# Kernel tuning notes

Measured on AMD Instinct MI355X. Metric: run time of the kernel, lower is better.

The kernel has to match this reference:

```python
import jax, jax.numpy as jnp
import numpy as np

B, T_ENC, D = 64, 512, 256
MEL, R = 80, 5
T_DEC = 200
IN = MEL * R  # 400


def _p(key, shape, scale):
    return jax.random.normal(key, shape, dtype=jnp.float32) * scale


def setup_inputs() -> dict:
    key = jax.random.key(0)
    ks = jax.random.split(key, 32)
    s = lambda fan: 1.0 / np.sqrt(fan)
    inp = {
        "enc_out": jax.random.normal(ks[0], (B, T_ENC, D), dtype=jnp.float32),
        "mel_in": jax.random.normal(ks[1], (B, T_DEC, IN), dtype=jnp.float32),
        # prenet: 400 -> 256 -> 128
        "prenet_w1": _p(ks[2], (IN, 256), s(IN)), "prenet_b1": jnp.zeros((256,), jnp.float32),
        "prenet_w2": _p(ks[3], (256, 128), s(256)), "prenet_b2": jnp.zeros((128,), jnp.float32),
        # attention GRUCell: input 128+256=384, hidden 256 (torch gate order r,z,n)
        "att_w_ih": _p(ks[4], (384, 768), s(384)), "att_w_hh": _p(ks[5], (256, 768), s(256)),
        "att_b_ih": jnp.zeros((768,), jnp.float32), "att_b_hh": jnp.zeros((768,), jnp.float32),
        # Bahdanau attention
        "mem_w": _p(ks[6], (D, 256), s(D)),
        "query_w": _p(ks[7], (256, 256), s(256)),
        "att_v": _p(ks[8], (256,), s(256)),
        # project_to_decoder_in: 512 -> 256
        "proj_w": _p(ks[9], (512, 256), s(512)), "proj_b": jnp.zeros((256,), jnp.float32),
        # 2 decoder GRUCells 256->256
        "dec1_w_ih": _p(ks[10], (256, 768), s(256)), "dec1_w_hh": _p(ks[11], (256, 768), s(256)),
        "dec1_b_ih": jnp.zeros((768,), jnp.float32), "dec1_b_hh": jnp.zeros((768,), jnp.float32),
        "dec2_w_ih": _p(ks[12], (256, 768), s(256)), "dec2_w_hh": _p(ks[13], (256, 768), s(256)),
        "dec2_b_ih": jnp.zeros((768,), jnp.float32), "dec2_b_hh": jnp.zeros((768,), jnp.float32),
        # proj_to_mel: 256 -> 400
        "mel_w": _p(ks[14], (256, IN), s(256)), "mel_b": jnp.zeros((IN,), jnp.float32),
    }
    return inp


def _gru(x, h, w_ih, w_hh, b_ih, b_hh):
    gi = x @ w_ih + b_ih
    gh = h @ w_hh + b_hh
    i_r, i_z, i_n = jnp.split(gi, 3, axis=-1)
    h_r, h_z, h_n = jnp.split(gh, 3, axis=-1)
    r = jax.nn.sigmoid(i_r + h_r)
    z = jax.nn.sigmoid(i_z + h_z)
    n = jnp.tanh(i_n + r * h_n)
    return (1.0 - z) * n + z * h


def reference(enc_out, mel_in, prenet_w1, prenet_b1, prenet_w2, prenet_b2,
              att_w_ih, att_w_hh, att_b_ih, att_b_hh, mem_w, query_w, att_v,
              proj_w, proj_b, dec1_w_ih, dec1_w_hh, dec1_b_ih, dec1_b_hh,
              dec2_w_ih, dec2_w_hh, dec2_b_ih, dec2_b_hh, mel_w, mel_b):
    b = enc_out.shape[0]
    # teacher forcing: go frame (zeros) then shifted mel targets
    dec_inputs = jnp.concatenate([jnp.zeros_like(mel_in[:, :1]), mel_in[:, :-1]], axis=1)  # [B,T,400]
    # prenet can be computed for all steps at once (input-only, state-free)
    x = jax.nn.relu(dec_inputs @ prenet_w1 + prenet_b1)
    x = jax.nn.relu(x @ prenet_w2 + prenet_b2)         # [B,T,128]
    xs = jnp.swapaxes(x, 0, 1)                          # [T,B,128]
    proc_mem = enc_out @ mem_w                          # [B,T_enc,256]
    zero = jnp.zeros((b, 256), enc_out.dtype)
    init = (zero, zero, zero, zero)  # att_hidden, context, dec_h1, dec_h2

    def step(carry, xt):
        att_h, ctx, h1, h2 = carry
        att_in = jnp.concatenate([xt, ctx], axis=-1)                 # [B,384]
        att_h = _gru(att_in, att_h, att_w_ih, att_w_hh, att_b_ih, att_b_hh)
        q = att_h @ query_w                                          # [B,256]
        e = jnp.tanh(proc_mem + q[:, None, :]) @ att_v               # [B,T_enc]
        a = jax.nn.softmax(e, axis=-1)
        ctx = jnp.einsum('bt,btd->bd', a, enc_out)                   # [B,256]
        d = jnp.concatenate([att_h, ctx], axis=-1) @ proj_w + proj_b # [B,256]
        h1 = _gru(d, h1, dec1_w_ih, dec1_w_hh, dec1_b_ih, dec1_b_hh)
        d = h1 + d
        h2 = _gru(d, h2, dec2_w_ih, dec2_w_hh, dec2_b_ih, dec2_b_hh)
        d = h2 + d
        out = d @ mel_w + mel_b                                      # [B,400]
        return (att_h, ctx, h1, h2), (out, a)

    _, (outs, aligns) = jax.lax.scan(step, init, xs)
    return jnp.swapaxes(outs, 0, 1), jnp.swapaxes(aligns, 0, 1)
```

## Files before the change

kernel.cpp:

```cpp
#include <hip/hip_runtime.h>
#include <hip/hip_bf16.h>

#define BB   64
#define TT   200
#define TE   512
#define DD   256
#define HH   256
#define GG   768
#define INW  400
#define PN1  256
#define PN2  128
#define GBLK 128
#define NG   (TT + 2)
#define SBE  (HH * BB)
#define CSC  2.8853900817779268f
#define L2E  1.4426950408889634f

typedef unsigned short ushortT;

__device__ __forceinline__ float blo(unsigned u) { return __uint_as_float(u << 16); }
__device__ __forceinline__ float bhi(unsigned u) { return __uint_as_float(u & 0xffff0000u); }
__device__ __forceinline__ float bf2f(ushortT u) { return __uint_as_float(((unsigned)u) << 16); }

__device__ __forceinline__ float sigmf_(float x) {
    return __builtin_amdgcn_rcpf(1.f + __builtin_amdgcn_exp2f(-L2E * x));
}
__device__ __forceinline__ float tanhf_(float x) {
    return 1.f - 2.f * __builtin_amdgcn_rcpf(__builtin_amdgcn_exp2f(CSC * x) + 1.f);
}
__device__ __forceinline__ float gru_h(float ir, float iz, float in_, float hr, float hz,
                                       float hn, float hp) {
    float r = sigmf_(ir + hr), z = sigmf_(iz + hz);
    float n = tanhf_(in_ + r * hn);
    return (1.f - z) * n + z * hp;
}

__device__ __forceinline__ void stS(float* p, float v) {
    __hip_atomic_store(p, v, __ATOMIC_RELAXED, __HIP_MEMORY_SCOPE_AGENT);
}

#define FMA4(acc, w4, x0, x1, x2, x3) \
    acc = fmaf(x0, w4.x, acc); acc = fmaf(x1, w4.y, acc); \
    acc = fmaf(x2, w4.z, acc); acc = fmaf(x3, w4.w, acc)

__device__ __forceinline__ void mv6(const float* __restrict__ st,
    const float* __restrict__ w0, const float* __restrict__ w1,
    const float* __restrict__ w2, const float* __restrict__ w3,
    const float* __restrict__ w4, const float* __restrict__ w5, int dims,
    float& a0, float& a1, float& a2, float& a3, float& a4, float& a5)
{
    for (int j = 0; j < dims; j += 4) {
        float x0 = st[(j + 0) * 64], x1 = st[(j + 1) * 64];
        float x2 = st[(j + 2) * 64], x3 = st[(j + 3) * 64];
        float4 w;
        w = *(const float4*)(w0 + j); FMA4(a0, w, x0, x1, x2, x3);
        w = *(const float4*)(w1 + j); FMA4(a1, w, x0, x1, x2, x3);
        w = *(const float4*)(w2 + j); FMA4(a2, w, x0, x1, x2, x3);
        w = *(const float4*)(w3 + j); FMA4(a3, w, x0, x1, x2, x3);
        w = *(const float4*)(w4 + j); FMA4(a4, w, x0, x1, x2, x3);
        w = *(const float4*)(w5 + j); FMA4(a5, w, x0, x1, x2, x3);
    }
}

__device__ __forceinline__ void mv4(const float* __restrict__ st,
    const float* __restrict__ w0, const float* __restrict__ w1,
    const float* __restrict__ w2, const float* __restrict__ w3, int dims,
    float& a0, float& a1, float& a2, float& a3)
{
    for (int j = 0; j < dims; j += 4) {
        float x0 = st[(j + 0) * 64], x1 = st[(j + 1) * 64];
        float x2 = st[(j + 2) * 64], x3 = st[(j + 3) * 64];
        float4 w;
        w = *(const float4*)(w0 + j); FMA4(a0, w, x0, x1, x2, x3);
        w = *(const float4*)(w1 + j); FMA4(a1, w, x0, x1, x2, x3);
        w = *(const float4*)(w2 + j); FMA4(a2, w, x0, x1, x2, x3);
        w = *(const float4*)(w3 + j); FMA4(a3, w, x0, x1, x2, x3);
    }
}

template<int AMODE, int SMODE, bool RELU, bool BIAS>
__global__ __launch_bounds__(256) void gemm_k(
    const float* __restrict__ A, const float* __restrict__ Bm,
    const float* __restrict__ bias, void* __restrict__ Cp,
    int M, int N, int K, int lda, int ldb)
{
    __shared__ __align__(16) float As[16][68];
    __shared__ __align__(16) float Bs[16][68];
    int tid = threadIdx.x;
    int m0 = blockIdx.y * 64, n0 = blockIdx.x * 64;
    int tx = tid & 15, ty = tid >> 4;
    float acc[4][4] = {};
    for (int k0 = 0; k0 < K; k0 += 16) {
        {
            int row = tid >> 2, kq = tid & 3;
            int gr = m0 + row;
            float4 a4;
            if (AMODE == 0) {
                a4 = *(const float4*)(A + (size_t)gr * lda + k0 + kq * 4);
            } else {
                int bb = gr / TT, t = gr % TT;
                if (t == 0) a4 = make_float4(0.f, 0.f, 0.f, 0.f);
                else a4 = *(const float4*)(A + ((size_t)bb * TT + (t - 1)) * INW + k0 + kq * 4);
            }
            As[kq * 4 + 0][row] = a4.x; As[kq * 4 + 1][row] = a4.y;
            As[kq * 4 + 2][row] = a4.z; As[kq * 4 + 3][row] = a4.w;
            int kk = tid >> 4, nq = tid & 15;
            int gc = n0 + nq * 4;
            float4 b4;
            if (gc + 3 < N) {
                b4 = *(const float4*)(Bm + (size_t)(k0 + kk) * ldb + gc);
            } else {
                b4.x = (gc + 0 < N) ? Bm[(size_t)(k0 + kk) * ldb + gc + 0] : 0.f;
                b4.y = (gc + 1 < N) ? Bm[(size_t)(k0 + kk) * ldb + gc + 1] : 0.f;
                b4.z = (gc + 2 < N) ? Bm[(size_t)(k0 + kk) * ldb + gc + 2] : 0.f;
                b4.w = (gc + 3 < N) ? Bm[(size_t)(k0 + kk) * ldb + gc + 3] : 0.f;
            }
            *(float4*)&Bs[kk][nq * 4] = b4;
        }
        __syncthreads();
#pragma unroll
        for (int kk = 0; kk < 16; ++kk) {
            float4 av = *(const float4*)&As[kk][ty * 4];
            float4 bv = *(const float4*)&Bs[kk][tx * 4];
            acc[0][0] = fmaf(av.x, bv.x, acc[0][0]); acc[0][1] = fmaf(av.x, bv.y, acc[0][1]);
            acc[0][2] = fmaf(av.x, bv.z, acc[0][2]); acc[0][3] = fmaf(av.x, bv.w, acc[0][3]);
            acc[1][0] = fmaf(av.y, bv.x, acc[1][0]); acc[1][1] = fmaf(av.y, bv.y, acc[1][1]);
            acc[1][2] = fmaf(av.y, bv.z, acc[1][2]); acc[1][3] = fmaf(av.y, bv.w, acc[1][3]);
            acc[2][0] = fmaf(av.z, bv.x, acc[2][0]); acc[2][1] = fmaf(av.z, bv.y, acc[2][1]);
            acc[2][2] = fmaf(av.z, bv.z, acc[2][2]); acc[2][3] = fmaf(av.z, bv.w, acc[2][3]);
            acc[3][0] = fmaf(av.w, bv.x, acc[3][0]); acc[3][1] = fmaf(av.w, bv.y, acc[3][1]);
            acc[3][2] = fmaf(av.w, bv.z, acc[3][2]); acc[3][3] = fmaf(av.w, bv.w, acc[3][3]);
        }
        __syncthreads();
    }
#pragma unroll
    for (int i = 0; i < 4; ++i) {
#pragma unroll
        for (int j = 0; j < 4; ++j) {
            int r = m0 + ty * 4 + i, c = n0 + tx * 4 + j;
            if (c >= N) continue;
            float v = acc[i][j];
            if (BIAS) v += bias[c];
            if (RELU) v = fmaxf(v, 0.f);
            if (SMODE == 0) ((float*)Cp)[(size_t)r * N + c] = v;
            else if (SMODE == 1) ((__hip_bfloat16*)Cp)[((size_t)(r % TT) * GG + c) * 64 + (r / TT)] = __float2bfloat16(v);
            else if (SMODE == 2) ((__hip_bfloat16*)Cp)[(size_t)r * N + c] = __float2bfloat16(v);
            else ((float*)Cp)[(size_t)c * M + r] = v;
        }
    }
}

template<bool BF16>
__global__ __launch_bounds__(256) void trans_k(const float* __restrict__ in, int IR, int IC,
                                               int rowoff, void* __restrict__ out)
{
    int idx = blockIdx.x * 256 + threadIdx.x;
    if (idx >= IR * IC) return;
    int c = idx / IR, r = idx % IR;
    float v = in[(size_t)(r + rowoff) * IC + c];
    if (BF16) ((__hip_bfloat16*)out)[idx] = __float2bfloat16(v);
    else ((float*)out)[idx] = v;
}

__global__ __launch_bounds__(256) void scale_k(const float* __restrict__ in,
                                               float* __restrict__ out, int n, float s)
{
    int i = blockIdx.x * 256 + threadIdx.x;
    if (i < n) out[i] = in[i] * s;
}

__global__ __launch_bounds__(256) void vprep_k(const float* __restrict__ v,
                                               float* __restrict__ vn2)
{
    int i = threadIdx.x;
    if (i < 256) vn2[i] = -2.f * v[i];
}

__global__ __launch_bounds__(256) void bfuse_k(const float* __restrict__ bih,
                                               const float* __restrict__ projb,
                                               const float* __restrict__ W, int N,
                                               float* __restrict__ out)
{
    int c = blockIdx.x * 256 + threadIdx.x;
    if (c >= N) return;
    float s = bih[c];
    for (int j = 0; j < 256; ++j) s = fmaf(projb[j], W[(size_t)j * N + c], s);
    out[c] = s;
}

__global__ __launch_bounds__(256) void outtr_k(const float* __restrict__ outsT,
                                               float* __restrict__ outs)
{
    int bid = blockIdx.x;
    int t = bid / 7, ct = bid % 7;
    int c0 = ct * 64, cw = (ct == 6) ? (INW - 384) : 64;
    int cwl = (cw == 64) ? 6 : 4;
    __shared__ float tile[64][65];
    int tid = threadIdx.x;
    for (int i = tid; i < cw * 64; i += 256) {
        int ci = i >> 6, bb = i & 63;
        tile[ci][bb] = outsT[((size_t)t * INW + c0 + ci) * 64 + bb];
    }
    __syncthreads();
    for (int i = tid; i < 64 * cw; i += 256) {
        int bb = i >> cwl, cc = i & (cw - 1);
        outs[((size_t)bb * TT + t) * INW + c0 + cc] = tile[cc][bb];
    }
}

__device__ __forceinline__ void gridbar(unsigned* cnt, unsigned bar) {
    __syncthreads();
    if (threadIdx.x == 0) {
        asm volatile("s_waitcnt vmcnt(0)" ::: "memory");
        __hip_atomic_fetch_add(cnt, 1u, __ATOMIC_RELAXED, __HIP_MEMORY_SCOPE_AGENT);
        unsigned target = bar * (unsigned)GBLK;
        while (__hip_atomic_load(cnt, __ATOMIC_RELAXED, __HIP_MEMORY_SCOPE_AGENT) < target) {
            __builtin_amdgcn_s_sleep(1);
        }
    }
    __syncthreads();
}

__device__ __forceinline__ float tpair(unsigned u32, int d, const float* qk,
                                       const float* vn2, float acc) {
    float xa = blo(u32) + qk[d];
    float xb = bhi(u32) + qk[d + 1];
    float ra = __builtin_amdgcn_rcpf(__builtin_amdgcn_exp2f(xa) + 1.f);
    float rb = __builtin_amdgcn_rcpf(__builtin_amdgcn_exp2f(xb) + 1.f);
    acc = fmaf(vn2[d], ra, acc);
    return fmaf(vn2[d + 1], rb, acc);
}

__global__ __launch_bounds__(512, 2) void mega_k(
    const ushortT* __restrict__ xgiB, const float* __restrict__ WihcT,
    const float* __restrict__ WhhT, const float* __restrict__ att_bhh,
    const float* __restrict__ F1T, const float* __restrict__ Whh1T,
    const float* __restrict__ bf1, const float* __restrict__ d1_bhh,
    const float* __restrict__ F2T, const float* __restrict__ Wih2T,
    const float* __restrict__ Whh2T, const float* __restrict__ b2c,
    const float* __restrict__ d2_bhh,
    const float* __restrict__ melT, const float* __restrict__ FMT,
    const float* __restrict__ bmc,
    const ushortT* __restrict__ WqT, const ushortT* __restrict__ pmB,
    const float* __restrict__ enc, const float* __restrict__ vn2g,
    float* __restrict__ Sh, float* __restrict__ Sc,
    float* __restrict__ S1, float* __restrict__ S2,
    float* __restrict__ outsT, float* __restrict__ aligns,
    unsigned* __restrict__ cnt)
{
    const int tid = threadIdx.x, bid = blockIdx.x;
    const int lane = tid & 63, wq = tid >> 6;
    __shared__ __align__(16) float smem[3104];
    float* part = smem;
    unsigned bar = 0;
    const int u0 = bid * 2;

    for (int t = 0; t < TT; ++t) {
        const float* hC  = Sh + (size_t)(t + 1) * SBE;  float* hN  = Sh + (size_t)(t + 2) * SBE;
        const float* cC  = Sc + (size_t)(t + 1) * SBE;  float* cN  = Sc + (size_t)(t + 2) * SBE;
        const float* h1C = S1 + (size_t)(t + 1) * SBE;  float* h1N = S1 + (size_t)(t + 2) * SBE;
        const float* h2C = S2 + (size_t)(t + 1) * SBE;  float* h2N = S2 + (size_t)(t + 2) * SBE;
        const ushortT* xgi_t = xgiB + (size_t)t * (GG * 64);

        {
            int q = wq & 3;
            const float* st = ((wq < 4) ? cC : hC) + (q * 64) * 64 + lane;
            const float* W  = (wq < 4) ? WihcT : WhhT;
            int ko = q * 64;
            float a0 = 0.f, a1 = 0.f, a2 = 0.f, a3 = 0.f, a4 = 0.f, a5 = 0.f;
            mv6(st,
                W + ((size_t)(0 * 256 + u0 + 0)) * 256 + ko,
                W + ((size_t)(0 * 256 + u0 + 1)) * 256 + ko,
                W + ((size_t)(1 * 256 + u0 + 0)) * 256 + ko,
                W + ((size_t)(1 * 256 + u0 + 1)) * 256 + ko,
                W + ((size_t)(2 * 256 + u0 + 0)) * 256 + ko,
                W + ((size_t)(2 * 256 + u0 + 1)) * 256 + ko,
                64, a0, a1, a2, a3, a4, a5);
            part[((wq * 2 + 0) * 3 + 0) * 64 + lane] = a0;
            part[((wq * 2 + 1) * 3 + 0) * 64 + lane] = a1;
            part[((wq * 2 + 0) * 3 + 1) * 64 + lane] = a2;
            part[((wq * 2 + 1) * 3 + 1) * 64 + lane] = a3;
            part[((wq * 2 + 0) * 3 + 2) * 64 + lane] = a4;
            part[((wq * 2 + 1) * 3 + 2) * 64 + lane] = a5;
            __syncthreads();
            if (wq < 2) {
                int uu = u0 + wq;
                float g_[6];
#pragma unroll
                for (int g = 0; g < 3; ++g) {
                    float si = 0.f, sh = 0.f;
#pragma unroll
                    for (int w = 0; w < 4; ++w) {
                        si += part[((w * 2 + wq) * 3 + g) * 64 + lane];
                        sh += part[(((w + 4) * 2 + wq) * 3 + g) * 64 + lane];
                    }
                    g_[g] = si; g_[3 + g] = sh;
                }
                float ir  = g_[0] + bf2f(xgi_t[(size_t)(0 * 256 + uu) * 64 + lane]);
                float iz  = g_[1] + bf2f(xgi_t[(size_t)(1 * 256 + uu) * 64 + lane]);
                float in_ = g_[2] + bf2f(xgi_t[(size_t)(2 * 256 + uu) * 64 + lane]);
                float hr = g_[3] + att_bhh[uu];
                float hz = g_[4] + att_bhh[256 + uu];
                float hn = g_[5] + att_bhh[512 + uu];
                float hp = hC[(size_t)uu * 64 + lane];
                stS(&hN[(size_t)uu * 64 + lane], gru_h(ir, iz, in_, hr, hz, hn, hp));
            }
        }
        gridbar(cnt, ++bar);

        if (bid < BB) {
            const int b = bid;
            float* hsh   = smem;
            float* qk    = smem + 256;
            float* vn2   = smem + 512;
            float* ash   = smem + 768;
            float* red   = smem + 1280;
            float* cpart = smem + 1312;
            if (tid < 256) { hsh[tid] = hN[(size_t)tid * 64 + b]; vn2[tid] = vn2g[tid]; }
            __syncthreads();
            if (tid < 256) {
                const ushortT* wr = WqT + (size_t)tid * 256;
                float acc = 0.f;
                for (int k = 0; k < 256; k += 8) {
                    uint4 w = *(const uint4*)(wr + k);
                    acc = fmaf(hsh[k + 0], blo(w.x), acc); acc = fmaf(hsh[k + 1], bhi(w.x), acc);
                    acc = fmaf(hsh[k + 2], blo(w.y), acc); acc = fmaf(hsh[k + 3], bhi(w.y), acc);
                    acc = fmaf(hsh[k + 4], blo(w.z), acc); acc = fmaf(hsh[k + 5], bhi(w.z), acc);
                    acc = fmaf(hsh[k + 6], blo(w.w), acc); acc = fmaf(hsh[k + 7], bhi(w.w), acc);
                }
                qk[tid] = acc * CSC;
            }
            __syncthreads();
            const ushortT* pr = pmB + ((size_t)b * TE + tid) * 256;
            float e = 0.f;
            for (int d = 0; d < 256; d += 8) {
                uint4 w = *(const uint4*)(pr + d);
                e = tpair(w.x, d + 0, qk, vn2, e);
                e = tpair(w.y, d + 2, qk, vn2, e);
                e = tpair(w.z, d + 4, qk, vn2, e);
                e = tpair(w.w, d + 6, qk, vn2, e);
            }
            float m = e;
            for (int o = 32; o; o >>= 1) m = fmaxf(m, __shfl_xor(m, o));
            if (lane == 0) red[wq] = m;
            __syncthreads();
            m = red[0];
            for (int i = 1; i < 8; ++i) m = fmaxf(m, red[i]);
            float pe = __builtin_amdgcn_exp2f((e - m) * L2E);
            float ssum = pe;
            for (int o = 32; o; o >>= 1) ssum += __shfl_xor(ssum, o);
            __syncthreads();
            if (lane == 0) red[wq] = ssum;
            __syncthreads();
            ssum = red[0] + red[1] + red[2] + red[3] + red[4] + red[5] + red[6] + red[7];
            float a = pe * __builtin_amdgcn_rcpf(ssum);
            ash[tid] = a;
            aligns[((size_t)b * TT + t) * TE + tid] = a;
            __syncthreads();
            int d = tid & 255, ph = tid >> 8;
            const float* er = enc + ((size_t)b * TE + ph * 256) * DD + d;
            const float* ap = ash + ph * 256;
            float acc = 0.f;
#pragma unroll 4
            for (int p = 0; p < 256; ++p) acc = fmaf(ap[p], er[(size_t)p * DD], acc);
            cpart[ph * 256 + d] = acc;
            __syncthreads();
            if (tid < 256) stS(&cN[(size_t)tid * 64 + b], cpart[tid] + cpart[256 + tid]);
        }
        gridbar(cnt, ++bar);

        {
            float a0 = 0.f, a1 = 0.f, a2 = 0.f, a3 = 0.f, a4 = 0.f, a5 = 0.f;
            if (wq < 4) {
                const float* st = ((wq < 2) ? hN : cN) + ((wq & 1) * 128) * 64 + lane;
                int ko = wq * 128;
                mv6(st,
                    F1T + ((size_t)(0 * 256 + u0 + 0)) * 512 + ko,
                    F1T + ((size_t)(0 * 256 + u0 + 1)) * 512 + ko,
                    F1T + ((size_t)(1 * 256 + u0 + 0)) * 512 + ko,
                    F1T + ((size_t)(1 * 256 + u0 + 1)) * 512 + ko,
                    F1T + ((size_t)(2 * 256 + u0 + 0)) * 512 + ko,
                    F1T + ((size_t)(2 * 256 + u0 + 1)) * 512 + ko,
                    128, a0, a1, a2, a3, a4, a5);
            } else {
                int q = wq - 4;
                const float* st = h1C + (q * 64) * 64 + lane;
                int ko = q * 64;
                mv6(st,
                    Whh1T + ((size_t)(0 * 256 + u0 + 0)) * 256 + ko,
                    Whh1T + ((size_t)(0 * 256 + u0 + 1)) * 256 + ko,
                    Whh1T + ((size_t)(1 * 256 + u0 + 0)) * 256 + ko,
                    Whh1T + ((size_t)(1 * 256 + u0 + 1)) * 256 + ko,
                    Whh1T + ((size_t)(2 * 256 + u0 + 0)) * 256 + ko,
                    Whh1T + ((size_t)(2 * 256 + u0 + 1)) * 256 + ko,
                    64, a0, a1, a2, a3, a4, a5);
            }
            part[((wq * 2 + 0) * 3 + 0) * 64 + lane] = a0;
            part[((wq * 2 + 1) * 3 + 0) * 64 + lane] = a1;
            part[((wq * 2 + 0) * 3 + 1) * 64 + lane] = a2;
            part[((wq * 2 + 1) * 3 + 1) * 64 + lane] = a3;
            part[((wq * 2 + 0) * 3 + 2) * 64 + lane] = a4;
            part[((wq * 2 + 1) * 3 + 2) * 64 + lane] = a5;
            __syncthreads();
            if (wq < 2) {
                int uu = u0 + wq;
                float ir = bf1[uu], iz = bf1[256 + uu], in_ = bf1[512 + uu];
                float hr = d1_bhh[uu], hz = d1_bhh[256 + uu], hn = d1_bhh[512 + uu];
#pragma unroll
                for (int w = 0; w < 4; ++w) {
                    ir  += part[((w * 2 + wq) * 3 + 0) * 64 + lane];
                    iz  += part[((w * 2 + wq) * 3 + 1) * 64 + lane];
                    in_ += part[((w * 2 + wq) * 3 + 2) * 64 + lane];
                    hr  += part[(((w + 4) * 2 + wq) * 3 + 0) * 64 + lane];
                    hz  += part[(((w + 4) * 2 + wq) * 3 + 1) * 64 + lane];
                    hn  += part[(((w + 4) * 2 + wq) * 3 + 2) * 64 + lane];
                }
                float hp = h1C[(size_t)uu * 64 + lane];
                stS(&h1N[(size_t)uu * 64 + lane], gru_h(ir, iz, in_, hr, hz, hn, hp));
            }
        }
        gridbar(cnt, ++bar);

        {
            const float* st; const float* W; int ko; size_t wstride;
            if (wq < 4)      { st = ((wq < 2) ? hN : cN) + ((wq & 1) * 128) * 64;
                               W = F2T;   ko = wq * 128;        wstride = 512; }
            else if (wq < 6) { st = h1N + ((wq & 1) * 128) * 64;
                               W = Wih2T; ko = (wq & 1) * 128;  wstride = 256; }
            else             { st = h2C + ((wq & 1) * 128) * 64;
                               W = Whh2T; ko = (wq & 1) * 128;  wstride = 256; }
            float a0 = 0.f, a1 = 0.f, a2 = 0.f, a3 = 0.f, a4 = 0.f, a5 = 0.f;
            mv6(st + lane,
                W + ((size_t)(0 * 256 + u0 + 0)) * wstride + ko,
                W + ((size_t)(0 * 256 + u0 + 1)) * wstride + ko,
                W + ((size_t)(1 * 256 + u0 + 0)) * wstride + ko,
                W + ((size_t)(1 * 256 + u0 + 1)) * wstride + ko,
                W + ((size_t)(2 * 256 + u0 + 0)) * wstride + ko,
                W + ((size_t)(2 * 256 + u0 + 1)) * wstride + ko,
                128, a0, a1, a2, a3, a4, a5);
            part[((wq * 2 + 0) * 3 + 0) * 64 + lane] = a0;
            part[((wq * 2 + 1) * 3 + 0) * 64 + lane] = a1;
            part[((wq * 2 + 0) * 3 + 1) * 64 + lane] = a2;
            part[((wq * 2 + 1) * 3 + 1) * 64 + lane] = a3;
            part[((wq * 2 + 0) * 3 + 2) * 64 + lane] = a4;
            part[((wq * 2 + 1) * 3 + 2) * 64 + lane] = a5;
            __syncthreads();
            if (wq < 2) {
                int uu = u0 + wq;
                float ir = b2c[uu], iz = b2c[256 + uu], in_ = b2c[512 + uu];
                float hr = d2_bhh[uu], hz = d2_bhh[256 + uu], hn = d2_bhh[512 + uu];
#pragma unroll
                for (int w = 0; w < 6; ++w) {
                    ir  += part[((w * 2 + wq) * 3 + 0) * 64 + lane];
                    iz  += part[((w * 2 + wq) * 3 + 1) * 64 + lane];
                    in_ += part[((w * 2 + wq) * 3 + 2) * 64 + lane];
                }
#pragma unroll
                for (int w = 6; w < 8; ++w) {
                    hr += part[((w * 2 + wq) * 3 + 0) * 64 + lane];
                    hz += part[((w * 2 + wq) * 3 + 1) * 64 + lane];
                    hn += part[((w * 2 + wq) * 3 + 2) * 64 + lane];
                }
                float hp = h2C[(size_t)uu * 64 + lane];
                stS(&h2N[(size_t)uu * 64 + lane], gru_h(ir, iz, in_, hr, hz, hn, hp));
            }
        }
        gridbar(cnt, ++bar);

        {
            int c0 = bid, half = wq & 1, ko = half * 128;
            int cA = c0,      wA = (cA < INW) ? cA : 0;
            int cB = c0+128,  wB = (cB < INW) ? cB : 0;
            int cC2 = c0+256, wC = (cC2 < INW) ? cC2 : 0;
            int cD = c0+384,  wD = (cD < INW) ? cD : 0;
            const float* st; const float* Wb; size_t wstride; int woff;
            if (wq < 2)      { st = h1N + ko * 64; Wb = melT; wstride = 256; woff = ko; }
            else if (wq < 4) { st = h2N + ko * 64; Wb = melT; wstride = 256; woff = ko; }
            else if (wq < 6) { st = hN + ko * 64;  Wb = FMT;  wstride = 512; woff = ko; }
            else             { st = cN + ko * 64;  Wb = FMT;  wstride = 512; woff = 256 + ko; }
            float a0 = 0.f, a1 = 0.f, a2 = 0.f, a3 = 0.f;
            mv4(st + lane,
                Wb + (size_t)wA * wstride + woff,
                Wb + (size_t)wB * wstride + woff,
                Wb + (size_t)wC * wstride + woff,
                Wb + (size_t)wD * wstride + woff,
                128, a0, a1, a2, a3);
            part[(wq * 4 + 0) * 64 + lane] = a0;
            part[(wq * 4 + 1) * 64 + lane] = a1;
            part[(wq * 4 + 2) * 64 + lane] = a2;
            part[(wq * 4 + 3) * 64 + lane] = a3;
            __syncthreads();
            if (wq < 4) {
                int c = c0 + 128 * wq;
                if (c < INW) {
                    float acc = bmc[c];
#pragma unroll
                    for (int w = 0; w < 8; ++w) acc += part[(w * 4 + wq) * 64 + lane];
                    outsT[((size_t)t * INW + c) * 64 + lane] = acc;
                }
            }
        }
        __syncthreads();
    }
}

extern "C" void kernel_launch(void* const* d_in, const int* in_sizes, int n_in,
                              void* d_out, int out_size, void* d_ws, size_t ws_size,
                              hipStream_t stream) {
    const float* enc     = (const float*)d_in[0];
    const float* mel     = (const float*)d_in[1];
    const float* pw1     = (const float*)d_in[2];
    const float* pb1     = (const float*)d_in[3];
    const float* pw2     = (const float*)d_in[4];
    const float* pb2     = (const float*)d_in[5];
    const float* att_wih = (const float*)d_in[6];
    const float* att_whh = (const float*)d_in[7];
    const float* att_bih = (const float*)d_in[8];
    const float* att_bhh = (const float*)d_in[9];
    const float* mem_w   = (const float*)d_in[10];
    const float* query_w = (const float*)d_in[11];
    const float* att_v   = (const float*)d_in[12];
    const float* proj_w  = (const float*)d_in[13];
    const float* proj_b  = (const float*)d_in[14];
    const float* d1_wih  = (const float*)d_in[15];
    const float* d1_whh  = (const float*)d_in[16];
    const float* d1_bih  = (const float*)d_in[17];
    const float* d1_bhh  = (const float*)d_in[18];
    const float* d2_wih  = (const float*)d_in[19];
    const float* d2_whh  = (const float*)d_in[20];
    const float* d2_bih  = (const float*)d_in[21];
    const float* d2_bhh  = (const float*)d_in[22];
    const float* mel_w   = (const float*)d_in[23];
    const float* mel_b   = (const float*)d_in[24];

    float* outs = (float*)d_out;
    float* aligns = outs + (size_t)BB * TT * INW;

    char* p = (char*)d_ws;
    auto take = [&](size_t bytes) -> char* {
        char* r = p;
        p += (bytes + 255) & ~(size_t)255;
        return r;
    };
    float* Sh = (float*)take((size_t)NG * SBE * 4);
    float* Sc = (float*)take((size_t)NG * SBE * 4);
    float* S1 = (float*)take((size_t)NG * SBE * 4);
    float* S2 = (float*)take((size_t)NG * SBE * 4);
    unsigned* cnt = (unsigned*)take(256);
    char* bufA = take((size_t)TT * INW * 64 * 4);
    float* X1 = (float*)bufA;
    float* X2 = (float*)(bufA + (size_t)BB * TT * PN1 * 4);
    float* outsT = (float*)bufA;
    ushortT* xgiB = (ushortT*)take((size_t)TT * GG * 64 * 2);
    __hip_bfloat16* pmB = (__hip_bfloat16*)take((size_t)BB * TE * DD * 2);
    float* WihcT = (float*)take((size_t)GG * 256 * 4);
    float* WhhT  = (float*)take((size_t)GG * 256 * 4);
    float* Whh1T = (float*)take((size_t)GG * 256 * 4);
    float* Whh2T = (float*)take((size_t)GG * 256 * 4);
    float* Wih2T = (float*)take((size_t)GG * 256 * 4);
    float* melT  = (float*)take((size_t)INW * 256 * 4);
    float* F1T   = (float*)take((size_t)GG * 512 * 4);
    float* F2T   = (float*)take((size_t)GG * 512 * 4);
    float* FMT   = (float*)take((size_t)INW * 512 * 4);
    __hip_bfloat16* WqT = (__hip_bfloat16*)take((size_t)256 * 256 * 2);
    float* memwS = (float*)take((size_t)DD * 256 * 4);
    float* bf1 = (float*)take(GG * 4);
    float* b2c = (float*)take(GG * 4);
    float* bmc = (float*)take(INW * 4);
    float* vn2g = (float*)take(256 * 4);

    (void)hipMemsetAsync(Sh, 0, 2 * SBE * 4, stream);
    (void)hipMemsetAsync(Sc, 0, 2 * SBE * 4, stream);
    (void)hipMemsetAsync(S1, 0, 2 * SBE * 4, stream);
    (void)hipMemsetAsync(S2, 0, 2 * SBE * 4, stream);
    (void)hipMemsetAsync(cnt, 0, 256, stream);

    trans_k<false><<<(256 * GG + 255) / 256, 256, 0, stream>>>(att_wih, 256, GG, 128, WihcT);
    trans_k<false><<<(256 * GG + 255) / 256, 256, 0, stream>>>(att_whh, 256, GG, 0, WhhT);
    trans_k<false><<<(256 * GG + 255) / 256, 256, 0, stream>>>(d1_whh, 256, GG, 0, Whh1T);
    trans_k<false><<<(256 * GG + 255) / 256, 256, 0, stream>>>(d2_whh, 256, GG, 0, Whh2T);
    trans_k<false><<<(256 * GG + 255) / 256, 256, 0, stream>>>(d2_wih, 256, GG, 0, Wih2T);
    trans_k<false><<<(256 * INW + 255) / 256, 256, 0, stream>>>(mel_w, 256, INW, 0, melT);
    trans_k<true><<<(256 * 256 + 255) / 256, 256, 0, stream>>>(query_w, 256, 256, 0, WqT);
    scale_k<<<(DD * 256 + 255) / 256, 256, 0, stream>>>(mem_w, memwS, DD * 256, CSC);
    vprep_k<<<1, 256, 0, stream>>>(att_v, vn2g);
    bfuse_k<<<3, 256, 0, stream>>>(d1_bih, proj_b, d1_wih, GG, bf1);
    bfuse_k<<<3, 256, 0, stream>>>(d2_bih, proj_b, d2_wih, GG, b2c);
    bfuse_k<<<2, 256, 0, stream>>>(mel_b, proj_b, mel_w, INW, bmc);

    gemm_k<1, 0, true, true><<<dim3(PN1 / 64, BB * TT / 64), 256, 0, stream>>>(
        mel, pw1, pb1, X1, BB * TT, PN1, INW, INW, PN1);
    gemm_k<0, 0, true, true><<<dim3(PN2 / 64, BB * TT / 64), 256, 0, stream>>>(
        X1, pw2, pb2, X2, BB * TT, PN2, PN1, PN1, PN2);
    gemm_k<0, 1, false, true><<<dim3(GG / 64, BB * TT / 64), 256, 0, stream>>>(
        X2, att_wih, att_bih, xgiB, BB * TT, GG, PN2, PN2, GG);
    gemm_k<0, 2, false, false><<<dim3(DD / 64, BB * TE / 64), 256, 0, stream>>>(
        enc, memwS, nullptr, pmB, BB * TE, DD, DD, DD, DD);
    gemm_k<0, 3, false, false><<<dim3(GG / 64, 512 / 64), 256, 0, stream>>>(
        proj_w, d1_wih, nullptr, F1T, 512, GG, 256, 256, GG);
    gemm_k<0, 3, false, false><<<dim3(GG / 64, 512 / 64), 256, 0, stream>>>(
        proj_w, d2_wih, nullptr, F2T, 512, GG, 256, 256, GG);
    gemm_k<0, 3, false, false><<<dim3((INW + 63) / 64, 512 / 64), 256, 0, stream>>>(
        proj_w, mel_w, nullptr, FMT, 512, INW, 256, 256, INW);

    mega_k<<<GBLK, 512, 0, stream>>>(
        xgiB, WihcT, WhhT, att_bhh,
        F1T, Whh1T, bf1, d1_bhh,
        F2T, Wih2T, Whh2T, b2c, d2_bhh,
        melT, FMT, bmc,
        (const ushortT*)WqT, (const ushortT*)pmB, enc, vn2g,
        Sh, Sc, S1, S2, outsT, aligns, cnt);

    outtr_k<<<TT * 7, 256, 0, stream>>>(outsT, outs);
}
```

Before: 19.58 ms.

## Overlap mel projection with attention GRU phase and use bf16 transposed encoder

Moves the per-step mel output projection out of its own grid-synchronised phase and into idle waves of the next step's attention-GRU phase, using the previous step's states, with a tail pass for the last step. The attention-GRU matvec is split across 4 waves instead of 8 to free those waves. The context reduction now reads a bf16, transposed copy of the encoder output with vectorised loads instead of strided fp32 loads. Loops get compile-time trip counts and unrolling, and the launch-bounds occupancy hint is dropped. The bf16 encoder lowers context precision, and the extra transpose kernel and buffer add preprocessing cost.

```diff
diff --git a/kernel.cpp b/kernel.cpp
--- a/kernel.cpp
+++ b/kernel.cpp
@@ -43,13 +43,15 @@
     acc = fmaf(x0, w4.x, acc); acc = fmaf(x1, w4.y, acc); \
     acc = fmaf(x2, w4.z, acc); acc = fmaf(x3, w4.w, acc)
 
+template<int DIMS>
 __device__ __forceinline__ void mv6(const float* __restrict__ st,
     const float* __restrict__ w0, const float* __restrict__ w1,
     const float* __restrict__ w2, const float* __restrict__ w3,
-    const float* __restrict__ w4, const float* __restrict__ w5, int dims,
+    const float* __restrict__ w4, const float* __restrict__ w5,
     float& a0, float& a1, float& a2, float& a3, float& a4, float& a5)
 {
-    for (int j = 0; j < dims; j += 4) {
+#pragma unroll 4
+    for (int j = 0; j < DIMS; j += 4) {
         float x0 = st[(j + 0) * 64], x1 = st[(j + 1) * 64];
         float x2 = st[(j + 2) * 64], x3 = st[(j + 3) * 64];
         float4 w;
@@ -62,12 +64,14 @@
     }
 }
 
+template<int DIMS>
 __device__ __forceinline__ void mv4(const float* __restrict__ st,
     const float* __restrict__ w0, const float* __restrict__ w1,
-    const float* __restrict__ w2, const float* __restrict__ w3, int dims,
+    const float* __restrict__ w2, const float* __restrict__ w3,
     float& a0, float& a1, float& a2, float& a3)
 {
-    for (int j = 0; j < dims; j += 4) {
+#pragma unroll 4
+    for (int j = 0; j < DIMS; j += 4) {
         float x0 = st[(j + 0) * 64], x1 = st[(j + 1) * 64];
         float x2 = st[(j + 2) * 64], x3 = st[(j + 3) * 64];
         float4 w;
@@ -188,6 +192,26 @@
     out[c] = s;
 }
 
+__global__ __launch_bounds__(256) void enct_k(const float* __restrict__ enc,
+                                              ushortT* __restrict__ encT)
+{
+    int bid = blockIdx.x;
+    int b = bid >> 6, pt = (bid >> 3) & 7, dt = bid & 7;
+    int p0 = pt * 64, d0 = dt * 32;
+    __shared__ ushortT tl[64][34];
+    int tid = threadIdx.x;
+    for (int i = tid; i < 64 * 32; i += 256) {
+        int dd = i & 31, pp = i >> 5;
+        float v = enc[((size_t)b * TE + p0 + pp) * DD + d0 + dd];
+        tl[pp][dd] = (ushortT)(__bfloat16_as_ushort(__float2bfloat16(v)));
+    }
+    __syncthreads();
+    for (int i = tid; i < 32 * 64; i += 256) {
+        int pp = i & 63, dd = i >> 6;
+        encT[((size_t)b * DD + d0 + dd) * TE + p0 + pp] = tl[pp][dd];
+    }
+}
+
 __global__ __launch_bounds__(256) void outtr_k(const float* __restrict__ outsT,
                                                float* __restrict__ outs)
 {
@@ -231,7 +255,7 @@
     return fmaf(vn2[d + 1], rb, acc);
 }
 
-__global__ __launch_bounds__(512, 2) void mega_k(
+__global__ __launch_bounds__(512) void mega_k(
     const ushortT* __restrict__ xgiB, const float* __restrict__ WihcT,
     const float* __restrict__ WhhT, const float* __restrict__ att_bhh,
     const float* __restrict__ F1T, const float* __restrict__ Whh1T,
@@ -242,7 +266,7 @@
     const float* __restrict__ melT, const float* __restrict__ FMT,
     const float* __restrict__ bmc,
     const ushortT* __restrict__ WqT, const ushortT* __restrict__ pmB,
-    const float* __restrict__ enc, const float* __restrict__ vn2g,
+    const ushortT* __restrict__ encT, const float* __restrict__ vn2g,
     float* __restrict__ Sh, float* __restrict__ Sc,
     float* __restrict__ S1, float* __restrict__ S2,
     float* __restrict__ outsT, float* __restrict__ aligns,
@@ -252,6 +276,7 @@
     const int lane = tid & 63, wq = tid >> 6;
     __shared__ __align__(16) float smem[3104];
     float* part = smem;
+    float* partB = smem + 1536;
     unsigned bar = 0;
     const int u0 = bid * 2;
 
@@ -263,47 +288,66 @@
         const ushortT* xgi_t = xgiB + (size_t)t * (GG * 64);
 
         {
-            int q = wq & 3;
-            const float* st = ((wq < 4) ? cC : hC) + (q * 64) * 64 + lane;
-            const float* W  = (wq < 4) ? WihcT : WhhT;
-            int ko = q * 64;
-            float a0 = 0.f, a1 = 0.f, a2 = 0.f, a3 = 0.f, a4 = 0.f, a5 = 0.f;
-            mv6(st,
-                W + ((size_t)(0 * 256 + u0 + 0)) * 256 + ko,
-                W + ((size_t)(0 * 256 + u0 + 1)) * 256 + ko,
-                W + ((size_t)(1 * 256 + u0 + 0)) * 256 + ko,
-                W + ((size_t)(1 * 256 + u0 + 1)) * 256 + ko,
-                W + ((size_t)(2 * 256 + u0 + 0)) * 256 + ko,
-                W + ((size_t)(2 * 256 + u0 + 1)) * 256 + ko,
-                64, a0, a1, a2, a3, a4, a5);
-            part[((wq * 2 + 0) * 3 + 0) * 64 + lane] = a0;
-            part[((wq * 2 + 1) * 3 + 0) * 64 + lane] = a1;
-            part[((wq * 2 + 0) * 3 + 1) * 64 + lane] = a2;
-            part[((wq * 2 + 1) * 3 + 1) * 64 + lane] = a3;
-            part[((wq * 2 + 0) * 3 + 2) * 64 + lane] = a4;
-            part[((wq * 2 + 1) * 3 + 2) * 64 + lane] = a5;
+            if (wq < 4) {
+                int role = wq >> 1, kh = wq & 1;
+                const float* st = (role ? hC : cC) + (kh * 128) * 64 + lane;
+                const float* W = role ? WhhT : WihcT;
+                int ko = kh * 128;
+                float a0 = 0.f, a1 = 0.f, a2 = 0.f, a3 = 0.f, a4 = 0.f, a5 = 0.f;
+                mv6<128>(st,
+                    W + ((size_t)(0 * 256 + u0 + 0)) * 256 + ko,
+                    W + ((size_t)(0 * 256 + u0 + 1)) * 256 + ko,
+                    W + ((size_t)(1 * 256 + u0 + 0)) * 256 + ko,
+                    W + ((size_t)(1 * 256 + u0 + 1)) * 256 + ko,
+                    W + ((size_t)(2 * 256 + u0 + 0)) * 256 + ko,
+                    W + ((size_t)(2 * 256 + u0 + 1)) * 256 + ko,
+                    a0, a1, a2, a3, a4, a5);
+                part[((wq * 2 + 0) * 3 + 0) * 64 + lane] = a0;
+                part[((wq * 2 + 1) * 3 + 0) * 64 + lane] = a1;
+                part[((wq * 2 + 0) * 3 + 1) * 64 + lane] = a2;
+                part[((wq * 2 + 1) * 3 + 1) * 64 + lane] = a3;
+                part[((wq * 2 + 0) * 3 + 2) * 64 + lane] = a4;
+                part[((wq * 2 + 1) * 3 + 2) * 64 + lane] = a5;
+            } else if (bid < 100 && t > 0) {
+                int c0 = bid * 4;
+                const float* st; const float* Wb; size_t ws; int woff;
+                if (wq == 4)      { st = h1C; Wb = melT; ws = 256; woff = 0; }
+                else if (wq == 5) { st = h2C; Wb = melT; ws = 256; woff = 0; }
+                else if (wq == 6) { st = hC;  Wb = FMT;  ws = 512; woff = 0; }
+                else              { st = cC;  Wb = FMT;  ws = 512; woff = 256; }
+                float a0 = 0.f, a1 = 0.f, a2 = 0.f, a3 = 0.f;
+                mv4<256>(st + lane,
+                    Wb + (size_t)(c0 + 0) * ws + woff,
+                    Wb + (size_t)(c0 + 1) * ws + woff,
+                    Wb + (size_t)(c0 + 2) * ws + woff,
+                    Wb + (size_t)(c0 + 3) * ws + woff,
+                    a0, a1, a2, a3);
+                partB[((wq - 4) * 4 + 0) * 64 + lane] = a0;
+                partB[((wq - 4) * 4 + 1) * 64 + lane] = a1;
+                partB[((wq - 4) * 4 + 2) * 64 + lane] = a2;
+                partB[((wq - 4) * 4 + 3) * 64 + lane] = a3;
+            }
             __syncthreads();
             if (wq < 2) {
                 int uu = u0 + wq;
-                float g_[6];
-#pragma unroll
-                for (int g = 0; g < 3; ++g) {
-                    float si = 0.f, sh = 0.f;
-#pragma unroll
-                    for (int w = 0; w < 4; ++w) {
-                        si += part[((w * 2 + wq) * 3 + g) * 64 + lane];
-                        sh += part[(((w + 4) * 2 + wq) * 3 + g) * 64 + lane];
-                    }
-                    g_[g] = si; g_[3 + g] = sh;
-                }
-                float ir  = g_[0] + bf2f(xgi_t[(size_t)(0 * 256 + uu) * 64 + lane]);
-                float iz  = g_[1] + bf2f(xgi_t[(size_t)(1 * 256 + uu) * 64 + lane]);
-                float in_ = g_[2] + bf2f(xgi_t[(size_t)(2 * 256 + uu) * 64 + lane]);
-                float hr = g_[3] + att_bhh[uu];
-                float hz = g_[4] + att_bhh[256 + uu];
-                float hn = g_[5] + att_bhh[512 + uu];
-                float hp = hC[(size_t)uu * 64 + lane];
+                float ir  = part[((0 * 2 + wq) * 3 + 0) * 64 + lane] + part[((1 * 2 + wq) * 3 + 0) * 64 + lane]
+                          + bf2f(xgi_t[(size_t)(0 * 256 + uu) * 64 + lane]);
+                float iz  = part[((0 * 2 + wq) * 3 + 1) * 64 + lane] + part[((1 * 2 + wq) * 3 + 1) * 64 + lane]
+                          + bf2f(xgi_t[(size_t)(1 * 256 + uu) * 64 + lane]);
+                float in_ = part[((0 * 2 + wq) * 3 + 2) * 64 + lane] + part[((1 * 2 + wq) * 3 + 2) * 64 + lane]
+                          + bf2f(xgi_t[(size_t)(2 * 256 + uu) * 64 + lane]);
+                float hr  = part[((2 * 2 + wq) * 3 + 0) * 64 + lane] + part[((3 * 2 + wq) * 3 + 0) * 64 + lane] + att_bhh[uu];
+                float hz  = part[((2 * 2 + wq) * 3 + 1) * 64 + lane] + part[((3 * 2 + wq) * 3 + 1) * 64 + lane] + att_bhh[256 + uu];
+                float hn  = part[((2 * 2 + wq) * 3 + 2) * 64 + lane] + part[((3 * 2 + wq) * 3 + 2) * 64 + lane] + att_bhh[512 + uu];
+                float hp  = hC[(size_t)uu * 64 + lane];
                 stS(&hN[(size_t)uu * 64 + lane], gru_h(ir, iz, in_, hr, hz, hn, hp));
+            }
+            if (wq >= 4 && bid < 100 && t > 0) {
+                int col = wq - 4, c = bid * 4 + col;
+                float acc = bmc[c];
+#pragma unroll
+                for (int w = 0; w < 4; ++w) acc += partB[(w * 4 + col) * 64 + lane];
+                outsT[((size_t)(t - 1) * INW + c) * 64 + lane] = acc;
             }
         }
         gridbar(cnt, ++bar);
@@ -321,6 +365,7 @@
             if (tid < 256) {
                 const ushortT* wr = WqT + (size_t)tid * 256;
                 float acc = 0.f;
+#pragma unroll
                 for (int k = 0; k < 256; k += 8) {
                     uint4 w = *(const uint4*)(wr + k);
                     acc = fmaf(hsh[k + 0], blo(w.x), acc); acc = fmaf(hsh[k + 1], bhi(w.x), acc);
@@ -333,6 +378,7 @@
             __syncthreads();
             const ushortT* pr = pmB + ((size_t)b * TE + tid) * 256;
             float e = 0.f;
+#pragma unroll 8
             for (int d = 0; d < 256; d += 8) {
                 uint4 w = *(const uint4*)(pr + d);
                 e = tpair(w.x, d + 0, qk, vn2, e);
@@ -358,11 +404,17 @@
             aligns[((size_t)b * TT + t) * TE + tid] = a;
             __syncthreads();
             int d = tid & 255, ph = tid >> 8;
-            const float* er = enc + ((size_t)b * TE + ph * 256) * DD + d;
+            const ushortT* er = encT + ((size_t)(b * DD + d)) * TE + ph * 256;
             const float* ap = ash + ph * 256;
             float acc = 0.f;
-#pragma unroll 4
-            for (int p = 0; p < 256; ++p) acc = fmaf(ap[p], er[(size_t)p * DD], acc);
+#pragma unroll
+            for (int p = 0; p < 256; p += 8) {
+                uint4 w = *(const uint4*)(er + p);
+                acc = fmaf(ap[p + 0], blo(w.x), acc); acc = fmaf(ap[p + 1], bhi(w.x), acc);
+                acc = fmaf(ap[p + 2], blo(w.y), acc); acc = fmaf(ap[p + 3], bhi(w.y), acc);
+                acc = fmaf(ap[p + 4], blo(w.z), acc); acc = fmaf(ap[p + 5], bhi(w.z), acc);
+                acc = fmaf(ap[p + 6], blo(w.w), acc); acc = fmaf(ap[p + 7], bhi(w.w), acc);
+            }
             cpart[ph * 256 + d] = acc;
             __syncthreads();
             if (tid < 256) stS(&cN[(size_t)tid * 64 + b], cpart[tid] + cpart[256 + tid]);
@@ -374,26 +426,26 @@
             if (wq < 4) {
                 const float* st = ((wq < 2) ? hN : cN) + ((wq & 1) * 128) * 64 + lane;
                 int ko = wq * 128;
-                mv6(st,
+                mv6<128>(st,
                     F1T + ((size_t)(0 * 256 + u0 + 0)) * 512 + ko,
                     F1T + ((size_t)(0 * 256 + u0 + 1)) * 512 + ko,
                     F1T + ((size_t)(1 * 256 + u0 + 0)) * 512 + ko,
                     F1T + ((size_t)(1 * 256 + u0 + 1)) * 512 + ko,
                     F1T + ((size_t)(2 * 256 + u0 + 0)) * 512 + ko,
                     F1T + ((size_t)(2 * 256 + u0 + 1)) * 512 + ko,
-                    128, a0, a1, a2, a3, a4, a5);
+                    a0, a1, a2, a3, a4, a5);
             } else {
                 int q = wq - 4;
                 const float* st = h1C + (q * 64) * 64 + lane;
                 int ko = q * 64;
-                mv6(st,
+                mv6<64>(st,
                     Whh1T + ((size_t)(0 * 256 + u0 + 0)) * 256 + ko,
                     Whh1T + ((size_t)(0 * 256 + u0 + 1)) * 256 + ko,
                     Whh1T + ((size_t)(1 * 256 + u0 + 0)) * 256 + ko,
                     Whh1T + ((size_t)(1 * 256 + u0 + 1)) * 256 + ko,
                     Whh1T + ((size_t)(2 * 256 + u0 + 0)) * 256 + ko,
                     Whh1T + ((size_t)(2 * 256 + u0 + 1)) * 256 + ko,
-                    64, a0, a1, a2, a3, a4, a5);
+                    a0, a1, a2, a3, a4, a5);
             }
             part[((wq * 2 + 0) * 3 + 0) * 64 + lane] = a0;
             part[((wq * 2 + 1) * 3 + 0) * 64 + lane] = a1;
@@ -430,14 +482,14 @@
             else             { st = h2C + ((wq & 1) * 128) * 64;
                                W = Whh2T; ko = (wq & 1) * 128;  wstride = 256; }
             float a0 = 0.f, a1 = 0.f, a2 = 0.f, a3 = 0.f, a4 = 0.f, a5 = 0.f;
-            mv6(st + lane,
+            mv6<128>(st + lane,
                 W + ((size_t)(0 * 256 + u0 + 0)) * wstride + ko,
                 W + ((size_t)(0 * 256 + u0 + 1)) * wstride + ko,
                 W + ((size_t)(1 * 256 + u0 + 0)) * wstride + ko,
                 W + ((size_t)(1 * 256 + u0 + 1)) * wstride + ko,
                 W + ((size_t)(2 * 256 + u0 + 0)) * wstride + ko,
                 W + ((size_t)(2 * 256 + u0 + 1)) * wstride + ko,
-                128, a0, a1, a2, a3, a4, a5);
+                a0, a1, a2, a3, a4, a5);
             part[((wq * 2 + 0) * 3 + 0) * 64 + lane] = a0;
             part[((wq * 2 + 1) * 3 + 0) * 64 + lane] = a1;
             part[((wq * 2 + 0) * 3 + 1) * 64 + lane] = a2;
@@ -466,41 +518,40 @@
             }
         }
         gridbar(cnt, ++bar);
-
-        {
-            int c0 = bid, half = wq & 1, ko = half * 128;
-            int cA = c0,      wA = (cA < INW) ? cA : 0;
-            int cB = c0+128,  wB = (cB < INW) ? cB : 0;
-            int cC2 = c0+256, wC = (cC2 < INW) ? cC2 : 0;
-            int cD = c0+384,  wD = (cD < INW) ? cD : 0;
-            const float* st; const float* Wb; size_t wstride; int woff;
-            if (wq < 2)      { st = h1N + ko * 64; Wb = melT; wstride = 256; woff = ko; }
-            else if (wq < 4) { st = h2N + ko * 64; Wb = melT; wstride = 256; woff = ko; }
-            else if (wq < 6) { st = hN + ko * 64;  Wb = FMT;  wstride = 512; woff = ko; }
-            else             { st = cN + ko * 64;  Wb = FMT;  wstride = 512; woff = 256 + ko; }
+    }
+
+    if (bid < 100) {
+        const float* hF  = Sh + (size_t)(TT + 1) * SBE;
+        const float* cF  = Sc + (size_t)(TT + 1) * SBE;
+        const float* h1F = S1 + (size_t)(TT + 1) * SBE;
+        const float* h2F = S2 + (size_t)(TT + 1) * SBE;
+        if (wq >= 4) {
+            int c0 = bid * 4;
+            const float* st; const float* Wb; size_t ws; int woff;
+            if (wq == 4)      { st = h1F; Wb = melT; ws = 256; woff = 0; }
+            else if (wq == 5) { st = h2F; Wb = melT; ws = 256; woff = 0; }
+            else if (wq == 6) { st = hF;  Wb = FMT;  ws = 512; woff = 0; }
+            else              { st = cF;  Wb = FMT;  ws = 512; woff = 256; }
             float a0 = 0.f, a1 = 0.f, a2 = 0.f, a3 = 0.f;
-            mv4(st + lane,
-                Wb + (size_t)wA * wstride + woff,
-                Wb + (size_t)wB * wstride + woff,
-                Wb + (size_t)wC * wstride + woff,
-                Wb + (size_t)wD * wstride + woff,
-                128, a0, a1, a2, a3);
-            part[(wq * 4 + 0) * 64 + lane] = a0;
-            part[(wq * 4 + 1) * 64 + lane] = a1;
-            part[(wq * 4 + 2) * 64 + lane] = a2;
-            part[(wq * 4 + 3) * 64 + lane] = a3;
-            __syncthreads();
-            if (wq < 4) {
-                int c = c0 + 128 * wq;
-                if (c < INW) {
-                    float acc = bmc[c];
-#pragma unroll
-                    for (int w = 0; w < 8; ++w) acc += part[(w * 4 + wq) * 64 + lane];
-                    outsT[((size_t)t * INW + c) * 64 + lane] = acc;
-                }
-            }
+            mv4<256>(st + lane,
+                Wb + (size_t)(c0 + 0) * ws + woff,
+                Wb + (size_t)(c0 + 1) * ws + woff,
+                Wb + (size_t)(c0 + 2) * ws + woff,
+                Wb + (size_t)(c0 + 3) * ws + woff,
+                a0, a1, a2, a3);
+            partB[((wq - 4) * 4 + 0) * 64 + lane] = a0;
+            partB[((wq - 4) * 4 + 1) * 64 + lane] = a1;
+            partB[((wq - 4) * 4 + 2) * 64 + lane] = a2;
+            partB[((wq - 4) * 4 + 3) * 64 + lane] = a3;
         }
         __syncthreads();
+        if (wq >= 4) {
+            int col = wq - 4, c = bid * 4 + col;
+            float acc = bmc[c];
+#pragma unroll
+            for (int w = 0; w < 4; ++w) acc += partB[(w * 4 + col) * 64 + lane];
+            outsT[((size_t)(TT - 1) * INW + c) * 64 + lane] = acc;
+        }
     }
 }
 
@@ -553,6 +604,7 @@
     float* outsT = (float*)bufA;
     ushortT* xgiB = (ushortT*)take((size_t)TT * GG * 64 * 2);
     __hip_bfloat16* pmB = (__hip_bfloat16*)take((size_t)BB * TE * DD * 2);
+    ushortT* encT = (ushortT*)take((size_t)BB * TE * DD * 2);
     float* WihcT = (float*)take((size_t)GG * 256 * 4);
     float* WhhT  = (float*)take((size_t)GG * 256 * 4);
     float* Whh1T = (float*)take((size_t)GG * 256 * 4);
@@ -584,6 +636,7 @@
     trans_k<true><<<(256 * 256 + 255) / 256, 256, 0, stream>>>(query_w, 256, 256, 0, WqT);
     scale_k<<<(DD * 256 + 255) / 256, 256, 0, stream>>>(mem_w, memwS, DD * 256, CSC);
     vprep_k<<<1, 256, 0, stream>>>(att_v, vn2g);
+    enct_k<<<64 * 64, 256, 0, stream>>>(enc, encT);
     bfuse_k<<<3, 256, 0, stream>>>(d1_bih, proj_b, d1_wih, GG, bf1);
     bfuse_k<<<3, 256, 0, stream>>>(d2_bih, proj_b, d2_wih, GG, b2c);
     bfuse_k<<<2, 256, 0, stream>>>(mel_b, proj_b, mel_w, INW, bmc);
@@ -608,7 +661,7 @@
         F1T, Whh1T, bf1, d1_bhh,
         F2T, Wih2T, Whh2T, b2c, d2_bhh,
         melT, FMT, bmc,
-        (const ushortT*)WqT, (const ushortT*)pmB, enc, vn2g,
+        (const ushortT*)WqT, (const ushortT*)pmB, encT, vn2g,
         Sh, Sc, S1, S2, outsT, aligns, cnt);
 
     outtr_k<<<TT * 7, 256, 0, stream>>>(outsT, outs);
```

Measured after the change: 17.36 ms. -11.3%, faster.
